# Optimization experiments

Hardware: AMD Instinct MI355X
Metric: run time of the kernel (lower is better)

## Reference

```python
import jax, jax.numpy as jnp
import numpy as np

N, E, D = 100000, 1600000, 128


def setup_inputs() -> dict:
    key = jax.random.key(0)
    ks = jax.random.split(key, 10)
    x = jax.random.normal(ks[0], (N, D), dtype=jnp.float32)
    edge_index = jax.random.randint(ks[1], (2, E), 0, N, dtype=jnp.int64)
    edge_weight = jax.random.uniform(ks[2], (E,), dtype=jnp.float32)
    s = 1.0 / np.sqrt(D)
    # PyG GraphConv params per layer: lin_rel (weight+bias), lin_root (weight, no bias)
    Wr0 = jax.random.uniform(ks[3], (D, D), jnp.float32, -s, s)
    br0 = jax.random.uniform(ks[4], (D,), jnp.float32, -s, s)
    Ws0 = jax.random.uniform(ks[5], (D, D), jnp.float32, -s, s)
    Wr1 = jax.random.uniform(ks[6], (D, D), jnp.float32, -s, s)
    br1 = jax.random.uniform(ks[7], (D,), jnp.float32, -s, s)
    Ws1 = jax.random.uniform(ks[8], (D, D), jnp.float32, -s, s)
    return {"x": x, "edge_index": edge_index, "edge_weight": edge_weight,
            "Wr0": Wr0, "br0": br0, "Ws0": Ws0,
            "Wr1": Wr1, "br1": br1, "Ws1": Ws1}


def _graph_conv(h, src, dst, Wr, br, Ws, ew=None):
    # message: gather source-node features (optionally scaled by edge weight)
    m = h[src]                                   # [E, D]
    if ew is not None:
        m = m * ew[:, None]
    agg = jax.ops.segment_sum(m, dst, num_segments=h.shape[0])  # [N, D] aggr='add'
    return agg @ Wr + br + h @ Ws                # lin_rel(agg) + lin_root(h)


def reference(x, edge_index, edge_weight, Wr0, br0, Ws0, Wr1, br1, Ws1):
    src, dst = edge_index[0], edge_index[1]
    h = jax.nn.relu(_graph_conv(x, src, dst, Wr0, br0, Ws0, edge_weight))
    h = jax.nn.relu(_graph_conv(h, src, dst, Wr1, br1, Ws1))
    return h
```

## Files before the change

### kernel.cpp

```cpp
#include <hip/hip_runtime.h>
#include <hip/hip_bf16.h>

#ifndef D_FEAT
#define D_FEAT 128
#endif

#define SLOTS 40
#define OVF_CAP 8192
#define NSCAT 2048

typedef __attribute__((ext_vector_type(8))) short bf16x8;
typedef __attribute__((ext_vector_type(4))) float f32x4;
typedef unsigned long long u64;

__device__ __forceinline__ unsigned short f2bf(float f) {
    union { float f; unsigned u; } v; v.f = f;
    unsigned r = v.u + 0x7FFF + ((v.u >> 16) & 1);
    return (unsigned short)(r >> 16);
}
__device__ __forceinline__ float bf2f_lo(unsigned u) {
    union { unsigned u; float f; } v; v.u = u << 16; return v.f;
}
__device__ __forceinline__ float bf2f_hi(unsigned u) {
    union { unsigned u; float f; } v; v.u = u & 0xFFFF0000u; return v.f;
}

__device__ __forceinline__ void pack_W_body(const float* __restrict__ Wr,
                                            const float* __restrict__ Ws,
                                            unsigned short* __restrict__ Wp,
                                            int t) {
    const int lane = t & 63;
    const int ct = (t >> 6) & 7;
    const int ks = t >> 9;
    const int col = ct * 16 + (lane & 15);
    const int kbase = ks * 32 + (lane >> 4) * 8;
    unsigned short v[8];
#pragma unroll
    for (int j = 0; j < 8; ++j) {
        const int k = kbase + j;
        const float w = (k < 128) ? Wr[(size_t)k * 128 + col]
                                  : Ws[(size_t)(k - 128) * 128 + col];
        v[j] = f2bf(w);
    }
    *reinterpret_cast<uint4*>(Wp + (size_t)t * 8) = *reinterpret_cast<uint4*>(v);
}

__global__ void __launch_bounds__(256)
prep_scatter(const int* __restrict__ src, const int* __restrict__ dst,
             const float* __restrict__ ew, int E, int N,
             int* __restrict__ pos, unsigned* __restrict__ ell,
             int* __restrict__ ovf_cnt, int4* __restrict__ ovf,
             const float* __restrict__ x, unsigned short* __restrict__ XH,
             int nconv,
             const float* __restrict__ Wr0, const float* __restrict__ Ws0,
             unsigned short* __restrict__ Wp0,
             const float* __restrict__ Wr1, const float* __restrict__ Ws1,
             unsigned short* __restrict__ Wp1) {
    const int b = blockIdx.x;
    if (b < NSCAT) {
        for (int i = b * 256 + threadIdx.x; i < E; i += NSCAT * 256) {
            const int d = dst[i];
            const int slot = atomicAdd(&pos[d], 1);
            if (slot < SLOTS) {
                const unsigned w12 = min(4095u, (unsigned)__float2int_rn(ew[i] * 4095.f));
                ell[(size_t)d * SLOTS + slot] = (unsigned)src[i] | (w12 << 20);
            } else {
                const int o = atomicAdd(ovf_cnt, 1);
                if (o < OVF_CAP)
                    ovf[o] = make_int4(src[i], d, __float_as_int(ew[i]), 0);
            }
        }
    } else if (b < NSCAT + nconv) {
        const int i = (b - NSCAT) * 256 + threadIdx.x;
        if (i >= N * 32) return;
        float4 v = reinterpret_cast<const float4*>(x)[i];
        unsigned lo = (unsigned)f2bf(v.x) | ((unsigned)f2bf(v.y) << 16);
        unsigned hi = (unsigned)f2bf(v.z) | ((unsigned)f2bf(v.w) << 16);
        reinterpret_cast<uint2*>(XH)[i] = make_uint2(lo, hi);
    } else if (b < NSCAT + nconv + 16) {
        pack_W_body(Wr0, Ws0, Wp0, (b - NSCAT - nconv) * 256 + threadIdx.x);
    } else {
        pack_W_body(Wr1, Ws1, Wp1, (b - NSCAT - nconv - 16) * 256 + threadIdx.x);
    }
}

template <bool WEIGHTED>
__global__ void ovf_fixup(const unsigned short* __restrict__ XH,
                          const int* __restrict__ ovf_cnt,
                          const int4* __restrict__ ovf,
                          unsigned short* __restrict__ AGG) {
    const int n = min(*ovf_cnt, OVF_CAP);
    const int lane = threadIdx.x;
    for (int e = 0; e < n; ++e) {
        const int4 r = ovf[e];
        const float w = WEIGHTED ? __int_as_float(r.z) : 1.f;
        const unsigned u = *reinterpret_cast<const unsigned*>(
            XH + (size_t)(unsigned)r.x * 128 + lane * 2);
        unsigned* pa = reinterpret_cast<unsigned*>(
            AGG + (size_t)r.y * 128 + lane * 2);
        const unsigned cur = *pa;
        const float ax = bf2f_lo(cur) + w * bf2f_lo(u);
        const float ay = bf2f_hi(cur) + w * bf2f_hi(u);
        *pa = (unsigned)f2bf(ax) | ((unsigned)f2bf(ay) << 16);
    }
}

template <bool WEIGHTED>
__global__ void __launch_bounds__(256)
gather_ell(const unsigned short* __restrict__ XH,
           const int* __restrict__ pos,
           const unsigned* __restrict__ ell,
           unsigned short* __restrict__ AGG,
           int N) {
    const int node = blockIdx.x * 4 + (threadIdx.x >> 6);
    const int lane = threadIdx.x & 63;
    if (node >= N) return;
    const int g = lane >> 4;
    const int c = lane & 15;

    const int deg = min(pos[node], SLOTS);
    const unsigned* ebase = ell + (size_t)node * SLOTS;

    float acc[8];
#pragma unroll
    for (int j = 0; j < 8; ++j) acc[j] = 0.f;

    auto body = [&](int i) {
        const unsigned r = ebase[i];
        const float w = WEIGHTED ? (float)(r >> 20) * (1.f / 4095.f) : 1.f;
        const uint4 v = *reinterpret_cast<const uint4*>(
            XH + (size_t)(r & 0xFFFFF) * 128 + c * 8);
        acc[0] += w * bf2f_lo(v.x); acc[1] += w * bf2f_hi(v.x);
        acc[2] += w * bf2f_lo(v.y); acc[3] += w * bf2f_hi(v.y);
        acc[4] += w * bf2f_lo(v.z); acc[5] += w * bf2f_hi(v.z);
        acc[6] += w * bf2f_lo(v.w); acc[7] += w * bf2f_hi(v.w);
    };

    int i = g;
    for (; i + 12 < deg; i += 16) { body(i); body(i + 4); body(i + 8); body(i + 12); }
    for (; i < deg; i += 4) body(i);

#pragma unroll
    for (int j = 0; j < 8; ++j) {
        acc[j] += __shfl_xor(acc[j], 16);
        acc[j] += __shfl_xor(acc[j], 32);
    }

    if (lane < 16) {
        uint4 o;
        o.x = (unsigned)f2bf(acc[0]) | ((unsigned)f2bf(acc[1]) << 16);
        o.y = (unsigned)f2bf(acc[2]) | ((unsigned)f2bf(acc[3]) << 16);
        o.z = (unsigned)f2bf(acc[4]) | ((unsigned)f2bf(acc[5]) << 16);
        o.w = (unsigned)f2bf(acc[6]) | ((unsigned)f2bf(acc[7]) << 16);
        *reinterpret_cast<uint4*>(AGG + (size_t)node * 128 + c * 8) = o;
    }
}

template <bool TO_BF16>
__global__ void __launch_bounds__(256)
gemm_mfma(const unsigned short* __restrict__ AGG,
          const unsigned short* __restrict__ XH,
          const unsigned short* __restrict__ Wp,
          const float* __restrict__ br,
          float* __restrict__ out,
          unsigned short* __restrict__ XHo,
          int N) {
    const int tid = threadIdx.x;
    const int wave = tid >> 6;
    const int lane = tid & 63;
    const int r0 = blockIdx.x * 128 + wave * 32;
    const int lk = (lane >> 4) * 8;

    int ra = r0 + (lane & 15);
    int rb = ra + 16;
    if (ra >= N) ra = N - 1;
    if (rb >= N) rb = N - 1;
    const unsigned short* paga = AGG + (size_t)ra * 128 + lk;
    const unsigned short* pagb = AGG + (size_t)rb * 128 + lk;
    const unsigned short* pxha = XH + (size_t)ra * 128 + lk;
    const unsigned short* pxhb = XH + (size_t)rb * 128 + lk;
    const unsigned short* pw = Wp + (size_t)lane * 8;

    f32x4 acc[2][8];
#pragma unroll
    for (int rt = 0; rt < 2; ++rt)
#pragma unroll
        for (int ct = 0; ct < 8; ++ct)
            acc[rt][ct] = (f32x4){0.f, 0.f, 0.f, 0.f};

#pragma unroll
    for (int ks = 0; ks < 8; ++ks) {
        const bf16x8 a0 = (ks < 4)
            ? *reinterpret_cast<const bf16x8*>(paga + ks * 32)
            : *reinterpret_cast<const bf16x8*>(pxha + (ks - 4) * 32);
        const bf16x8 a1 = (ks < 4)
            ? *reinterpret_cast<const bf16x8*>(pagb + ks * 32)
            : *reinterpret_cast<const bf16x8*>(pxhb + (ks - 4) * 32);
#pragma unroll
        for (int ct = 0; ct < 8; ++ct) {
            const bf16x8 b = *reinterpret_cast<const bf16x8*>(pw + (((ks << 3) + ct) << 9));
            acc[0][ct] = __builtin_amdgcn_mfma_f32_16x16x32_bf16(a0, b, acc[0][ct], 0, 0, 0);
            acc[1][ct] = __builtin_amdgcn_mfma_f32_16x16x32_bf16(a1, b, acc[1][ct], 0, 0, 0);
        }
    }

    const int crow = (lane >> 4) * 4;
    const int ccol = lane & 15;
#pragma unroll
    for (int ct = 0; ct < 8; ++ct) {
        const int col = ct * 16 + ccol;
        const float bias = br[col];
#pragma unroll
        for (int rt = 0; rt < 2; ++rt) {
#pragma unroll
            for (int reg = 0; reg < 4; ++reg) {
                const int row = r0 + rt * 16 + crow + reg;
                if (row >= N) continue;
                const float v = fmaxf(acc[rt][ct][reg] + bias, 0.f);
                if (TO_BF16) {
                    XHo[(size_t)row * 128 + col] = f2bf(v);
                } else {
                    out[(size_t)row * 128 + col] = v;
                }
            }
        }
    }
}

extern "C" void kernel_launch(void* const* d_in, const int* in_sizes, int n_in,
                              void* d_out, int out_size, void* d_ws, size_t ws_size,
                              hipStream_t stream) {
    const float* x  = (const float*)d_in[0];
    const int*   ei = (const int*)d_in[1];
    const float* ew = (const float*)d_in[2];
    const float* Wr0 = (const float*)d_in[3];
    const float* br0 = (const float*)d_in[4];
    const float* Ws0 = (const float*)d_in[5];
    const float* Wr1 = (const float*)d_in[6];
    const float* br1 = (const float*)d_in[7];
    const float* Ws1 = (const float*)d_in[8];

    const int N = in_sizes[0] / D_FEAT;
    const int E = in_sizes[1] / 2;
    const int* src = ei;
    const int* dst = ei + E;

    char* w = (char*)d_ws;
    auto carve = [&](size_t bytes) { char* p = w; w += (bytes + 15) & ~(size_t)15; return p; };
    unsigned short* XH  = (unsigned short*)carve((size_t)N * 128 * 2);
    unsigned short* AGG = (unsigned short*)carve((size_t)N * 128 * 2);
    unsigned short* Wp0 = (unsigned short*)carve(256 * 128 * 2);
    unsigned short* Wp1 = (unsigned short*)carve(256 * 128 * 2);
    int*      pos     = (int*)     carve((size_t)N * 4);
    int*      ovf_cnt = (int*)     carve(16);
    int4*     ovf     = (int4*)    carve((size_t)OVF_CAP * 16);
    unsigned* ell     = (unsigned*)carve((size_t)N * SLOTS * 4);

    float* out = (float*)d_out;

    const int nconv = (N * 32 + 255) / 256;
    const int gather_blocks = (N + 3) / 4;
    const int gemm_blocks = (N + 127) / 128;

    hipMemsetAsync(pos, 0, (size_t)N * 4, stream);
    hipMemsetAsync(ovf_cnt, 0, 4, stream);
    prep_scatter<<<NSCAT + nconv + 32, 256, 0, stream>>>(
        src, dst, ew, E, N, pos, ell, ovf_cnt, ovf,
        x, XH, nconv, Wr0, Ws0, Wp0, Wr1, Ws1, Wp1);

    gather_ell<true><<<gather_blocks, 256, 0, stream>>>(XH, pos, ell, AGG, N);
    ovf_fixup<true><<<1, 64, 0, stream>>>(XH, ovf_cnt, ovf, AGG);
    gemm_mfma<true><<<gemm_blocks, 256, 0, stream>>>(AGG, XH, Wp0, br0, nullptr, XH, N);

    gather_ell<false><<<gather_blocks, 256, 0, stream>>>(XH, pos, ell, AGG, N);
    ovf_fixup<false><<<1, 64, 0, stream>>>(XH, ovf_cnt, ovf, AGG);
    gemm_mfma<false><<<gemm_blocks, 256, 0, stream>>>(AGG, XH, Wp1, br1, out, nullptr, N);
}
```

Before: 326.4 us.

## Replace direct ELL scatter with two-pass bucketed staging by destination block

Edge scattering into the ELL table is split into two passes. Each chunk first counts edges per 256-node destination bucket in shared memory, reserves space with one global atomic per bucket, and writes packed 64-bit records into a staging area that reuses the output buffer. A second kernel then builds the ELL rows bucket by bucket, so the per-node atomics and writes fall in a localized region. SLOTS also grows from 40 to 48. This adds an extra kernel launch and another pass over the staged data, and overflow edges now carry the quantized weight.

```diff
diff --git a/kernel.cpp b/kernel.cpp
--- a/kernel.cpp
+++ b/kernel.cpp
@@ -5,9 +5,11 @@
 #define D_FEAT 128
 #endif
 
-#define SLOTS 40
+#define SLOTS 48
 #define OVF_CAP 8192
-#define NSCAT 2048
+#define BWN 256
+#define CAPB 4608
+#define CHUNK_A 4096
 
 typedef __attribute__((ext_vector_type(8))) short bf16x8;
 typedef __attribute__((ext_vector_type(4))) float f32x4;
@@ -45,42 +47,98 @@
     *reinterpret_cast<uint4*>(Wp + (size_t)t * 8) = *reinterpret_cast<uint4*>(v);
 }
 
+__global__ void init_gcur(int* __restrict__ gcur, int NB) {
+    const int t = blockIdx.x * blockDim.x + threadIdx.x;
+    if (t < NB) gcur[t] = t * CAPB;
+}
+
 __global__ void __launch_bounds__(256)
-prep_scatter(const int* __restrict__ src, const int* __restrict__ dst,
-             const float* __restrict__ ew, int E, int N,
-             int* __restrict__ pos, unsigned* __restrict__ ell,
-             int* __restrict__ ovf_cnt, int4* __restrict__ ovf,
-             const float* __restrict__ x, unsigned short* __restrict__ XH,
-             int nconv,
-             const float* __restrict__ Wr0, const float* __restrict__ Ws0,
-             unsigned short* __restrict__ Wp0,
-             const float* __restrict__ Wr1, const float* __restrict__ Ws1,
-             unsigned short* __restrict__ Wp1) {
+prep_split(const int* __restrict__ src, const int* __restrict__ dst,
+           const float* __restrict__ ew, int E, int N, int NB, int nchunkA,
+           int* __restrict__ gcur, u64* __restrict__ stg,
+           int* __restrict__ ovf_cnt, int4* __restrict__ ovf,
+           const float* __restrict__ x, unsigned short* __restrict__ XH,
+           int nconv,
+           const float* __restrict__ Wr0, const float* __restrict__ Ws0,
+           unsigned short* __restrict__ Wp0,
+           const float* __restrict__ Wr1, const float* __restrict__ Ws1,
+           unsigned short* __restrict__ Wp1) {
     const int b = blockIdx.x;
-    if (b < NSCAT) {
-        for (int i = b * 256 + threadIdx.x; i < E; i += NSCAT * 256) {
-            const int d = dst[i];
-            const int slot = atomicAdd(&pos[d], 1);
-            if (slot < SLOTS) {
+    if (b < nchunkA) {
+        __shared__ int cnt[512];
+        __shared__ int base[512];
+        for (int t = threadIdx.x; t < NB; t += 256) cnt[t] = 0;
+        __syncthreads();
+        const int lo = b * CHUNK_A;
+        const int hi = min(lo + CHUNK_A, E);
+        int dreg[CHUNK_A / 256];
+#pragma unroll
+        for (int k = 0; k < CHUNK_A / 256; ++k) {
+            const int i = lo + k * 256 + threadIdx.x;
+            int d = -1;
+            if (i < hi) d = dst[i];
+            dreg[k] = d;
+            if (d >= 0) atomicAdd(&cnt[d >> 8], 1);
+        }
+        __syncthreads();
+        for (int t = threadIdx.x; t < NB; t += 256) {
+            base[t] = atomicAdd(&gcur[t], cnt[t]);
+            cnt[t] = 0;
+        }
+        __syncthreads();
+#pragma unroll
+        for (int k = 0; k < CHUNK_A / 256; ++k) {
+            const int i = lo + k * 256 + threadIdx.x;
+            const int d = dreg[k];
+            if (d < 0) continue;
+            const int bk = d >> 8;
+            const int off = atomicAdd(&cnt[bk], 1);
+            const int gi = base[bk] + off;
+            if (gi < (bk + 1) * CAPB) {
                 const unsigned w12 = min(4095u, (unsigned)__float2int_rn(ew[i] * 4095.f));
-                ell[(size_t)d * SLOTS + slot] = (unsigned)src[i] | (w12 << 20);
+                stg[gi] = (u64)(unsigned)src[i] | ((u64)(unsigned)(d & 255) << 20)
+                        | ((u64)w12 << 28);
             } else {
                 const int o = atomicAdd(ovf_cnt, 1);
                 if (o < OVF_CAP)
                     ovf[o] = make_int4(src[i], d, __float_as_int(ew[i]), 0);
             }
         }
-    } else if (b < NSCAT + nconv) {
-        const int i = (b - NSCAT) * 256 + threadIdx.x;
+    } else if (b < nchunkA + nconv) {
+        const int i = (b - nchunkA) * 256 + threadIdx.x;
         if (i >= N * 32) return;
         float4 v = reinterpret_cast<const float4*>(x)[i];
         unsigned lo = (unsigned)f2bf(v.x) | ((unsigned)f2bf(v.y) << 16);
         unsigned hi = (unsigned)f2bf(v.z) | ((unsigned)f2bf(v.w) << 16);
         reinterpret_cast<uint2*>(XH)[i] = make_uint2(lo, hi);
-    } else if (b < NSCAT + nconv + 16) {
-        pack_W_body(Wr0, Ws0, Wp0, (b - NSCAT - nconv) * 256 + threadIdx.x);
+    } else if (b < nchunkA + nconv + 16) {
+        pack_W_body(Wr0, Ws0, Wp0, (b - nchunkA - nconv) * 256 + threadIdx.x);
     } else {
-        pack_W_body(Wr1, Ws1, Wp1, (b - NSCAT - nconv - 16) * 256 + threadIdx.x);
+        pack_W_body(Wr1, Ws1, Wp1, (b - nchunkA - nconv - 16) * 256 + threadIdx.x);
+    }
+}
+
+__global__ void __launch_bounds__(256)
+build_ell(const u64* __restrict__ stg, const int* __restrict__ gcur,
+          int NB, int* __restrict__ pos, unsigned* __restrict__ ell,
+          int* __restrict__ ovf_cnt, int4* __restrict__ ovf) {
+    const int b = blockIdx.x;
+    const int beg = b * CAPB;
+    const int end = min(gcur[b], (b + 1) * CAPB);
+    for (int i = beg + threadIdx.x; i < end; i += 256) {
+        const u64 r = stg[i];
+        const int d = b * BWN + (int)((r >> 20) & 0xFF);
+        const int slot = atomicAdd(&pos[d], 1);
+        if (slot < SLOTS) {
+            ell[(size_t)d * SLOTS + slot] =
+                (unsigned)(r & 0xFFFFF) | ((unsigned)(r >> 28) << 20);
+        } else {
+            const int o = atomicAdd(ovf_cnt, 1);
+            if (o < OVF_CAP) {
+                const float w = (float)((r >> 28) & 0xFFF) * (1.f / 4095.f);
+                ovf[o] = make_int4((int)(r & 0xFFFFF), d, __float_as_int(w), 0);
+            }
+        }
     }
 }
 
@@ -244,6 +302,7 @@
     const int E = in_sizes[1] / 2;
     const int* src = ei;
     const int* dst = ei + E;
+    const int NB = (N + BWN - 1) / BWN;
 
     char* w = (char*)d_ws;
     auto carve = [&](size_t bytes) { char* p = w; w += (bytes + 15) & ~(size_t)15; return p; };
@@ -253,20 +312,27 @@
     unsigned short* Wp1 = (unsigned short*)carve(256 * 128 * 2);
     int*      pos     = (int*)     carve((size_t)N * 4);
     int*      ovf_cnt = (int*)     carve(16);
+    int*      gcur    = (int*)     carve(512 * 4);
     int4*     ovf     = (int4*)    carve((size_t)OVF_CAP * 16);
     unsigned* ell     = (unsigned*)carve((size_t)N * SLOTS * 4);
 
     float* out = (float*)d_out;
+    u64* stg = (u64*)d_out;
 
     const int nconv = (N * 32 + 255) / 256;
+    const int nchunkA = (E + CHUNK_A - 1) / CHUNK_A;
     const int gather_blocks = (N + 3) / 4;
     const int gemm_blocks = (N + 127) / 128;
 
     hipMemsetAsync(pos, 0, (size_t)N * 4, stream);
     hipMemsetAsync(ovf_cnt, 0, 4, stream);
-    prep_scatter<<<NSCAT + nconv + 32, 256, 0, stream>>>(
-        src, dst, ew, E, N, pos, ell, ovf_cnt, ovf,
+    init_gcur<<<2, 256, 0, stream>>>(gcur, NB);
+
+    prep_split<<<nchunkA + nconv + 32, 256, 0, stream>>>(
+        src, dst, ew, E, N, NB, nchunkA, gcur, stg, ovf_cnt, ovf,
         x, XH, nconv, Wr0, Ws0, Wp0, Wr1, Ws1, Wp1);
+
+    build_ell<<<NB, 256, 0, stream>>>(stg, gcur, NB, pos, ell, ovf_cnt, ovf);
 
     gather_ell<true><<<gather_blocks, 256, 0, stream>>>(XH, pos, ell, AGG, N);
     ovf_fixup<true><<<1, 64, 0, stream>>>(XH, ovf_cnt, ovf, AGG);
```

New measurement: 280.1 us, median of 2. 14.2% less time.
